# Kernel tuning notes

Hardware: AMD Instinct MI355X
Metric: run time of the kernel (lower is better)

## Reference

```python
import jax, jax.numpy as jnp
import numpy as np

N = 100000   # nodes
E = 1600000  # edges (avg degree 16)
F = 64       # input feature dim
H = 64       # hidden dim
O = 64       # conv output dim
C = 2        # channels (x.shape[1])
S = 1000     # number of subgraphs
M = 64       # nodes per subgraph
MH = 128     # MLP hidden
OUT = 1      # MLP output


def setup_inputs() -> dict:
    key = jax.random.key(0)
    ks = jax.random.split(key, 16)
    x = jax.random.normal(ks[0], (N, C, F), jnp.float32)
    edge_index = jax.random.randint(ks[1], (2, E), 0, N, dtype=jnp.int32)
    edge_weight = jax.random.uniform(ks[2], (E,), jnp.float32)
    subG_node = jax.random.randint(ks[3], (S, M), 0, N, dtype=jnp.int32)
    s1 = 1.0 / np.sqrt(F)
    s2 = 1.0 / np.sqrt(H)
    sm1 = 1.0 / np.sqrt(O)
    sm2 = 1.0 / np.sqrt(MH)
    return {
        "x": x,
        "edge_index": edge_index,
        "edge_weight": edge_weight,
        "subG_node": subG_node,
        "W1": jax.random.normal(ks[4], (F, H), jnp.float32) * s1,
        "b1": jnp.zeros((H,), jnp.float32),
        "gn_w": jnp.ones((H,), jnp.float32),
        "gn_b": jnp.zeros((H,), jnp.float32),
        "gn_ms": jnp.ones((H,), jnp.float32),
        "W2": jax.random.normal(ks[5], (H, O), jnp.float32) * s2,
        "b2": jnp.zeros((O,), jnp.float32),
        "mW1": jax.random.normal(ks[6], (O, MH), jnp.float32) * sm1,
        "mb1": jnp.zeros((MH,), jnp.float32),
        "mW2": jax.random.normal(ks[7], (MH, OUT), jnp.float32) * sm2,
        "mb2": jnp.zeros((OUT,), jnp.float32),
    }


def _graph_norm(h, w, b, ms, eps=1e-5):
    # PyG GraphNorm over all nodes (single graph): per-feature stats
    mean = jnp.mean(h, axis=0, keepdims=True)
    out = h - ms * mean
    var = jnp.mean(out * out, axis=0, keepdims=True)
    return w * out * jax.lax.rsqrt(var + eps) + b


def _gcn_layer(h, src, dst, norm, self_norm, W, b, n):
    # GCNConv: h' = D^-1/2 (A + I) D^-1/2 (h @ W) + b
    hw = h @ W                                   # [N, out]
    msg = norm[:, None] * hw[src]                # [E, out] gather
    agg = jax.ops.segment_sum(msg, dst, num_segments=n)  # scatter-add
    agg = agg + self_norm[:, None] * hw          # self-loop term
    return agg + b


def reference(x, edge_index, edge_weight, subG_node,
              W1, b1, gn_w, gn_b, gn_ms, W2, b2, mW1, mb1, mW2, mb2):
    n = x.shape[0]
    src, dst = edge_index[0], edge_index[1]
    # symmetric GCN normalization with self-loops of weight 1
    deg = jax.ops.segment_sum(edge_weight, dst, num_segments=n) + 1.0
    dinv = jax.lax.rsqrt(deg)
    norm = dinv[src] * edge_weight * dinv[dst]   # [E]
    self_norm = dinv * dinv                      # [N]

    def conv_channel(xc):  # xc: [N, F]
        h = _gcn_layer(xc, src, dst, norm, self_norm, W1, b1, n)
        h = _graph_norm(h, gn_w, gn_b, gn_ms)
        h = jax.nn.relu(h)
        return _gcn_layer(h, src, dst, norm, self_norm, W2, b2, n)

    emb = jax.vmap(conv_channel, in_axes=1, out_axes=1)(x)  # [N, C, O]
    emb = jnp.mean(emb, axis=1)                              # [N, O]
    # subgraph pooling: sp @ emb == sum of member-node embeddings
    pooled = jnp.sum(emb[subG_node], axis=1)                 # [S, O]
    h = jax.nn.relu(pooled @ mW1 + mb1)
    return h @ mW2 + mb2                                     # [S, 1]
```

## Files before the change

kernel.cpp:

```cpp
#include <hip/hip_runtime.h>
#include <hip/hip_fp16.h>

#define NNODES 100000
#define NEDGES 1600000
#define NSUB   1000
#define MSUB   64
#define MHID   128

#define WSHIFT 9
#define WIN    512
#define NWIN   ((NNODES + 511) >> 9)
#define NBLK   256
#define CHUNK  (NEDGES / NBLK)

typedef _Float16 f16x8 __attribute__((ext_vector_type(8)));
typedef float    f32x4 __attribute__((ext_vector_type(4)));


__global__ __launch_bounds__(256) void k_hist(const int* __restrict__ dst,
                                              int* __restrict__ block_counts) {
    __shared__ int hist[NWIN];
    int t = threadIdx.x, b = blockIdx.x;
    for (int i = t; i < NWIN; i += 256) hist[i] = 0;
    __syncthreads();
    int e0 = b * CHUNK;
    for (int e = e0 + t; e < e0 + CHUNK; e += 256)
        atomicAdd(&hist[dst[e] >> WSHIFT], 1);
    __syncthreads();
    for (int i = t; i < NWIN; i += 256) block_counts[b * NWIN + i] = hist[i];
}

__global__ __launch_bounds__(256) void k_winsum(const int* __restrict__ block_counts,
                                                int* __restrict__ win_total) {
    __shared__ int red[256];
    int t = threadIdx.x, w = blockIdx.x;
    red[t] = block_counts[t * NWIN + w];
    __syncthreads();
    for (int off = 128; off > 0; off >>= 1) {
        if (t < off) red[t] += red[t + off];
        __syncthreads();
    }
    if (t == 0) win_total[w] = red[0];
}

__global__ __launch_bounds__(256) void k_scan(const int* __restrict__ win_total,
                                              int* __restrict__ win_base,
                                              float* __restrict__ stats,
                                              int2* __restrict__ edges) {
    __shared__ int arr[256];
    int t = threadIdx.x;
    int own = (t < NWIN) ? win_total[t] : 0;
    arr[t] = own;
    __syncthreads();
    for (int off = 1; off < 256; off <<= 1) {
        int v = (t >= off) ? arr[t - off] : 0;
        __syncthreads();
        arr[t] += v;
        __syncthreads();
    }
    if (t < NWIN) win_base[t] = arr[t] - own;
    if (t == NWIN - 1) win_base[NWIN] = arr[t];
    stats[t] = 0.0f; stats[t + 256] = 0.0f;
    if (t < 16) edges[NEDGES + t] = make_int2(0, 0);
}

__global__ __launch_bounds__(64) void k_scan2(const int* __restrict__ block_counts,
                                              const int* __restrict__ win_base,
                                              int* __restrict__ block_off) {
    int w = blockIdx.x, lane = threadIdx.x;
    int c[4];
    int lsum = 0;
    #pragma unroll
    for (int i = 0; i < 4; i++) {
        c[i] = block_counts[(lane * 4 + i) * NWIN + w];
        lsum += c[i];
    }
    int incl = lsum;
    #pragma unroll
    for (int off = 1; off < 64; off <<= 1) {
        int u = __shfl_up(incl, off, 64);
        if (lane >= off) incl += u;
    }
    int run = win_base[w] + incl - lsum;
    #pragma unroll
    for (int i = 0; i < 4; i++) {
        block_off[(lane * 4 + i) * NWIN + w] = run;
        run += c[i];
    }
}

__global__ __launch_bounds__(256) void k_scatter(const int* __restrict__ src,
                                                 const int* __restrict__ dst,
                                                 const float* __restrict__ ew,
                                                 const int* __restrict__ block_off,
                                                 int2* __restrict__ esw) {
    __shared__ int myoff[NWIN];
    int t = threadIdx.x, b = blockIdx.x;
    for (int i = t; i < NWIN; i += 256) myoff[i] = block_off[b * NWIN + i];
    __syncthreads();
    int e0 = b * CHUNK;
    for (int e = e0 + t; e < e0 + CHUNK; e += 256) {
        int d = dst[e];
        int w = d >> WSHIFT;
        int pos = atomicAdd(&myoff[w], 1);
        int dl = d - (w << WSHIFT);
        esw[pos] = make_int2((dl << 17) | src[e], __float_as_int(ew[e]));
    }
}

__global__ __launch_bounds__(256) void k_fill2(const int* __restrict__ win_base,
                                               const int2* __restrict__ esw,
                                               int2* __restrict__ edges,
                                               int* __restrict__ row_ptr,
                                               int* __restrict__ cnt,
                                               float* __restrict__ dinv) {
    __shared__ int   cnt_l[WIN];
    __shared__ int   sc[WIN];
    __shared__ int   fill_l[WIN];
    __shared__ float degw[WIN];
    int t = threadIdx.x, w = blockIdx.x;
    #pragma unroll
    for (int i = t; i < WIN; i += 256) { cnt_l[i] = 0; fill_l[i] = 0; degw[i] = 0.f; }
    __syncthreads();
    int e0 = win_base[w], e1 = win_base[w + 1];
    for (int e = e0 + t; e < e1; e += 256) {
        int2 v = esw[e];
        int dl = ((unsigned)v.x) >> 17;
        atomicAdd(&cnt_l[dl], 1);
        atomicAdd(&degw[dl], __int_as_float(v.y));
    }
    __syncthreads();
    sc[t] = cnt_l[t]; sc[t + 256] = cnt_l[t + 256];
    __syncthreads();
    for (int off = 1; off < WIN; off <<= 1) {
        int v0 = (t >= off) ? sc[t - off] : 0;
        int v1 = (t + 256 >= off) ? sc[t + 256 - off] : 0;
        __syncthreads();
        sc[t] += v0; sc[t + 256] += v1;
        __syncthreads();
    }
    sc[t]       = e0 + sc[t]       - cnt_l[t];
    sc[t + 256] = e0 + sc[t + 256] - cnt_l[t + 256];
    __syncthreads();
    for (int e = e0 + t; e < e1; e += 256) {
        int2 v = esw[e];
        int dl = ((unsigned)v.x) >> 17;
        int pos = sc[dl] + atomicAdd(&fill_l[dl], 1);
        edges[pos] = make_int2(v.x & 0x1FFFF, v.y);
    }
    __syncthreads();
    #pragma unroll
    for (int i = t; i < WIN; i += 256) {
        int node = (w << WSHIFT) + i;
        if (node < NNODES) {
            row_ptr[node] = sc[i];
            cnt[node]     = cnt_l[i];
            dinv[node]    = rsqrtf(degw[i] + 1.0f);
        }
    }
}


template <bool TR>
__global__ __launch_bounds__(256) void k_gemm(const void* __restrict__ Xv,
                                              const float* __restrict__ Wg,
                                              const float* __restrict__ dinv,
                                              _Float16* __restrict__ Y,
                                              const float* __restrict__ Acoef,
                                              const float* __restrict__ Bcoef) {
    __shared__ __align__(16) _Float16 ob[4][16 * 72];
    int t = threadIdx.x;
    int wave = t >> 6, lane = t & 63;
    int m = lane & 15, q = lane >> 4;

    f16x8 bf[2][4];
    #pragma unroll
    for (int kb = 0; kb < 2; kb++)
        #pragma unroll
        for (int nt = 0; nt < 4; nt++)
            #pragma unroll
            for (int j = 0; j < 8; j++)
                bf[kb][nt][j] = (_Float16)Wg[(kb * 32 + q * 8 + j) * 64 + nt * 16 + m];

    float ca[16], cb[16];
    if constexpr (TR) {
        int c = m & 1;
        #pragma unroll
        for (int kb = 0; kb < 2; kb++)
            #pragma unroll
            for (int j = 0; j < 8; j++) {
                int k = kb * 32 + q * 8 + j;
                ca[kb * 8 + j] = Acoef[c * 64 + k];
                cb[kb * 8 + j] = Bcoef[c * 64 + k];
            }
    }

    int tile = blockIdx.x * 4 + wave;
    int row0 = tile * 16;

    f16x8 af[2];
    if constexpr (!TR) {
        const float* xp = (const float*)Xv + (size_t)(row0 + m) * 64;
        #pragma unroll
        for (int kb = 0; kb < 2; kb++) {
            float4 u0 = *(const float4*)(xp + kb * 32 + q * 8);
            float4 u1 = *(const float4*)(xp + kb * 32 + q * 8 + 4);
            af[kb][0] = (_Float16)u0.x; af[kb][1] = (_Float16)u0.y;
            af[kb][2] = (_Float16)u0.z; af[kb][3] = (_Float16)u0.w;
            af[kb][4] = (_Float16)u1.x; af[kb][5] = (_Float16)u1.y;
            af[kb][6] = (_Float16)u1.z; af[kb][7] = (_Float16)u1.w;
        }
    } else {
        const _Float16* xp = (const _Float16*)Xv + (size_t)(row0 + m) * 64;
        #pragma unroll
        for (int kb = 0; kb < 2; kb++) {
            f16x8 v = *(const f16x8*)(xp + kb * 32 + q * 8);
            #pragma unroll
            for (int j = 0; j < 8; j++) {
                float f = (float)v[j];
                f = fmaxf(ca[kb * 8 + j] * f + cb[kb * 8 + j], 0.0f);
                af[kb][j] = (_Float16)f;
            }
        }
    }

    f32x4 acc[4];
    #pragma unroll
    for (int nt = 0; nt < 4; nt++) {
        acc[nt] = (f32x4){0.f, 0.f, 0.f, 0.f};
        acc[nt] = __builtin_amdgcn_mfma_f32_16x16x32_f16(af[0], bf[0][nt], acc[nt], 0, 0, 0);
        acc[nt] = __builtin_amdgcn_mfma_f32_16x16x32_f16(af[1], bf[1][nt], acc[nt], 0, 0, 0);
    }

    float dv[4];
    #pragma unroll
    for (int i = 0; i < 4; i++) dv[i] = dinv[(row0 + q * 4 + i) >> 1];

    _Float16* obw = ob[wave];
    #pragma unroll
    for (int nt = 0; nt < 4; nt++)
        #pragma unroll
        for (int i = 0; i < 4; i++)
            obw[(q * 4 + i) * 72 + nt * 16 + m] = (_Float16)(acc[nt][i] * dv[i]);
    __syncthreads();

    _Float16* yp = Y + (size_t)row0 * 64;
    #pragma unroll
    for (int s = 0; s < 2; s++) {
        int c8 = s * 64 + lane;
        int r = c8 >> 3, cg = c8 & 7;
        uint4 v = *(const uint4*)(obw + r * 72 + cg * 8);
        *(uint4*)(yp + (size_t)r * 64 + cg * 8) = v;
    }
}


__global__ __launch_bounds__(256) void k_prop(const __half* __restrict__ hw,
                                              const float* __restrict__ bias,
                                              const float* __restrict__ dinv,
                                              const int* __restrict__ row_ptr,
                                              const int* __restrict__ cnt,
                                              const int2* __restrict__ edges,
                                              __half* __restrict__ agg) {
    int t = threadIdx.x;
    int lane = t & 63;
    int n = __builtin_amdgcn_readfirstlane(blockIdx.x * 4 + (t >> 6));
    if (n >= NNODES) return;

    int f = lane * 2;
    int feat = f & 63;

    float2 bv = *(const float2*)(bias + feat);
    float dv = dinv[n];
    float2 self = __half22float2(*(const __half2*)(hw + (size_t)n * 128 + f));
    float acc0 = self.x;
    float acc1 = self.y;

    int start = row_ptr[n];
    int cn    = cnt[n];
    const unsigned long long* pp = (const unsigned long long*)(edges + start);

    for (int p = 0; p < cn; p += 16) {
        unsigned long long e[16];
        #pragma unroll
        for (int i = 0; i < 16; i++) e[i] = __builtin_nontemporal_load(pp + p + i);
        float2 h[16];
        #pragma unroll
        for (int i = 0; i < 16; i++) {
            int s = (int)(e[i] & 0x1FFFFu);
            h[i] = __half22float2(*(const __half2*)(hw + (size_t)s * 128 + f));
        }
        #pragma unroll
        for (int i = 0; i < 16; i++) {
            float w = ((p + i) < cn) ? __int_as_float((int)(e[i] >> 32)) : 0.0f;
            acc0 += w * h[i].x;
            acc1 += w * h[i].y;
        }
    }

    *(__half2*)(agg + (size_t)n * 128 + f) =
        __floats2half2_rn(dv * acc0 + bv.x, dv * acc1 + bv.y);
}


__global__ __launch_bounds__(256) void k_stats(const __half* __restrict__ agg,
                                               float* __restrict__ stats) {
    __shared__ float ls[16][128];
    __shared__ float lq[16][128];
    int t = threadIdx.x;
    int cb = (t & 15) * 8;
    int rg = t >> 4;
    float s[8], q[8];
    #pragma unroll
    for (int i = 0; i < 8; i++) { s[i] = 0.f; q[i] = 0.f; }
    for (int r = blockIdx.x * 16 + rg; r < NNODES; r += gridDim.x * 16) {
        uint4 u = *(const uint4*)(agg + (size_t)r * 128 + cb);
        const __half2* h2 = (const __half2*)&u;
        #pragma unroll
        for (int i = 0; i < 4; i++) {
            float2 v = __half22float2(h2[i]);
            s[2*i]   += v.x; q[2*i]   += v.x * v.x;
            s[2*i+1] += v.y; q[2*i+1] += v.y * v.y;
        }
    }
    #pragma unroll
    for (int i = 0; i < 8; i++) { ls[rg][cb + i] = s[i]; lq[rg][cb + i] = q[i]; }
    __syncthreads();
    if (t < 128) {
        float a = 0.f, b = 0.f;
        #pragma unroll
        for (int g = 0; g < 16; g++) { a += ls[g][t]; b += lq[g][t]; }
        atomicAdd(&stats[t], a);
        atomicAdd(&stats[128 + t], b);
    }
}

__global__ void k_coef(float* stats, const float* __restrict__ gn_w,
                       const float* __restrict__ gn_b, const float* __restrict__ gn_ms) {
    int col = threadIdx.x;
    float inv_n = 1.0f / (float)NNODES;
    float mean = stats[col] * inv_n;
    float eh2  = stats[128 + col] * inv_n;
    int f = col & 63;
    float ms = gn_ms[f];
    float var = eh2 - 2.0f * ms * mean * mean + ms * ms * mean * mean;
    float A = gn_w[f] * rsqrtf(var + 1e-5f);
    stats[256 + col] = A;
    stats[384 + col] = gn_b[f] - A * ms * mean;
}


__global__ __launch_bounds__(128) void k_head(const __half* __restrict__ agg,
                                              const int* __restrict__ subg,
                                              const float* __restrict__ mW1,
                                              const float* __restrict__ mb1,
                                              const float* __restrict__ mW2,
                                              const float* __restrict__ mb2,
                                              float* __restrict__ out) {
    __shared__ float pl[128];
    __shared__ float red[128];
    int s = blockIdx.x, t = threadIdx.x;
    int j = t & 63, half = t >> 6;
    const int* idx = subg + s * 64;
    float acc = 0.f;
    for (int m = half * 32; m < half * 32 + 32; m++) {
        int n = idx[m];
        acc += 0.5f * (__half2float(agg[(size_t)n * 128 + j]) +
                       __half2float(agg[(size_t)n * 128 + 64 + j]));
    }
    pl[half * 64 + j] = acc;
    __syncthreads();
    if (t < 64) pl[t] += pl[64 + t];
    __syncthreads();
    float h = mb1[t];
    #pragma unroll
    for (int k = 0; k < 64; k++) h += pl[k] * mW1[k * 128 + t];
    h = fmaxf(h, 0.0f);
    red[t] = h * mW2[t];
    __syncthreads();
    for (int off = 64; off > 0; off >>= 1) {
        if (t < off) red[t] += red[t + off];
        __syncthreads();
    }
    if (t == 0) out[s] = red[0] + mb2[0];
}


extern "C" void kernel_launch(void* const* d_in, const int* in_sizes, int n_in,
                              void* d_out, int out_size, void* d_ws, size_t ws_size,
                              hipStream_t stream) {
    const float* x     = (const float*)d_in[0];
    const int*   ei    = (const int*)d_in[1];
    const float* ew    = (const float*)d_in[2];
    const int*   subg  = (const int*)d_in[3];
    const float* W1    = (const float*)d_in[4];
    const float* b1    = (const float*)d_in[5];
    const float* gn_w  = (const float*)d_in[6];
    const float* gn_b  = (const float*)d_in[7];
    const float* gn_ms = (const float*)d_in[8];
    const float* W2    = (const float*)d_in[9];
    const float* b2    = (const float*)d_in[10];
    const float* mW1   = (const float*)d_in[11];
    const float* mb1   = (const float*)d_in[12];
    const float* mW2   = (const float*)d_in[13];
    const float* mb2   = (const float*)d_in[14];
    float* out = (float*)d_out;

    char* w = (char*)d_ws;
    size_t off = 0;
    auto alloc = [&](size_t bytes) {
        void* p = w + off;
        off = (off + bytes + 255) & ~(size_t)255;
        return p;
    };
    float*  dinv      = (float*) alloc((size_t)NNODES * 4);
    int*    cnt       = (int*)   alloc((size_t)NNODES * 4);
    int*    row_ptr   = (int*)   alloc((size_t)NNODES * 4);
    int2*   edges     = (int2*)  alloc(((size_t)NEDGES + 16) * 8);
    int2*   esw       = (int2*)  alloc((size_t)NEDGES * 8);
    __half* hw        = (__half*)alloc((size_t)NNODES * 128 * 2);
    __half* agg       = (__half*)alloc((size_t)NNODES * 128 * 2);
    float*  stats     = (float*) alloc(512 * 4);
    int*    block_counts = (int*)alloc((size_t)NBLK * NWIN * 4);
    int*    block_off    = (int*)alloc((size_t)NBLK * NWIN * 4);
    int*    win_total    = (int*)alloc(NWIN * 4);
    int*    win_base     = (int*)alloc((NWIN + 1) * 4);

    const int* src = ei;
    const int* dst = ei + NEDGES;

    k_hist   <<<NBLK, 256, 0, stream>>>(dst, block_counts);
    k_winsum <<<NWIN, 256, 0, stream>>>(block_counts, win_total);
    k_scan   <<<1, 256, 0, stream>>>(win_total, win_base, stats, edges);
    k_scan2  <<<NWIN, 64, 0, stream>>>(block_counts, win_base, block_off);
    k_scatter<<<NBLK, 256, 0, stream>>>(src, dst, ew, block_off, esw);
    k_fill2  <<<NWIN, 256, 0, stream>>>(win_base, esw, edges, row_ptr, cnt, dinv);

    k_gemm<false><<<3125, 256, 0, stream>>>(x, W1, dinv, (_Float16*)hw, nullptr, nullptr);
    k_prop<<<25000, 256, 0, stream>>>(hw, b1, dinv, row_ptr, cnt, edges, agg);

    k_stats<<<512, 256, 0, stream>>>(agg, stats);
    k_coef<<<1, 128, 0, stream>>>(stats, gn_w, gn_b, gn_ms);

    k_gemm<true><<<3125, 256, 0, stream>>>(agg, W2, dinv, (_Float16*)hw, stats + 256, stats + 384);
    k_prop<<<25000, 256, 0, stream>>>(hw, b2, dinv, row_ptr, cnt, edges, agg);

    k_head<<<NSUB, 128, 0, stream>>>(agg, subg, mW1, mb1, mW2, mb2, out);
}
```

Measured before the change: 382.9 us.

## Pack edges into 32-bit with quantized weights and merge offset kernels

```diff
diff --git a/kernel.cpp b/kernel.cpp
--- a/kernel.cpp
+++ b/kernel.cpp
@@ -18,9 +18,11 @@
 
 
 __global__ __launch_bounds__(256) void k_hist(const int* __restrict__ dst,
-                                              int* __restrict__ block_counts) {
+                                              int* __restrict__ block_counts,
+                                              int* __restrict__ cursor) {
     __shared__ int hist[NWIN];
     int t = threadIdx.x, b = blockIdx.x;
+    if (b == 0 && t == 0) *cursor = 0;
     for (int i = t; i < NWIN; i += 256) hist[i] = 0;
     __syncthreads();
     int e0 = b * CHUNK;
@@ -30,62 +32,37 @@
     for (int i = t; i < NWIN; i += 256) block_counts[b * NWIN + i] = hist[i];
 }
 
-__global__ __launch_bounds__(256) void k_winsum(const int* __restrict__ block_counts,
-                                                int* __restrict__ win_total) {
+__global__ __launch_bounds__(256) void k_off(const int* __restrict__ block_counts,
+                                             int* __restrict__ cursor,
+                                             int* __restrict__ win_base,
+                                             int* __restrict__ win_lim,
+                                             int* __restrict__ block_off,
+                                             float* __restrict__ stats,
+                                             unsigned* __restrict__ edges) {
+    __shared__ int arr[256];
     __shared__ int red[256];
+    __shared__ int base_s;
     int t = threadIdx.x, w = blockIdx.x;
-    red[t] = block_counts[t * NWIN + w];
+    int own = block_counts[t * NWIN + w];
+    arr[t] = own; red[t] = own;
     __syncthreads();
     for (int off = 128; off > 0; off >>= 1) {
         if (t < off) red[t] += red[t + off];
         __syncthreads();
     }
-    if (t == 0) win_total[w] = red[0];
-}
-
-__global__ __launch_bounds__(256) void k_scan(const int* __restrict__ win_total,
-                                              int* __restrict__ win_base,
-                                              float* __restrict__ stats,
-                                              int2* __restrict__ edges) {
-    __shared__ int arr[256];
-    int t = threadIdx.x;
-    int own = (t < NWIN) ? win_total[t] : 0;
-    arr[t] = own;
-    __syncthreads();
+    if (t == 0) base_s = atomicAdd(cursor, red[0]);
     for (int off = 1; off < 256; off <<= 1) {
         int v = (t >= off) ? arr[t - off] : 0;
         __syncthreads();
         arr[t] += v;
         __syncthreads();
     }
-    if (t < NWIN) win_base[t] = arr[t] - own;
-    if (t == NWIN - 1) win_base[NWIN] = arr[t];
-    stats[t] = 0.0f; stats[t + 256] = 0.0f;
-    if (t < 16) edges[NEDGES + t] = make_int2(0, 0);
-}
-
-__global__ __launch_bounds__(64) void k_scan2(const int* __restrict__ block_counts,
-                                              const int* __restrict__ win_base,
-                                              int* __restrict__ block_off) {
-    int w = blockIdx.x, lane = threadIdx.x;
-    int c[4];
-    int lsum = 0;
-    #pragma unroll
-    for (int i = 0; i < 4; i++) {
-        c[i] = block_counts[(lane * 4 + i) * NWIN + w];
-        lsum += c[i];
-    }
-    int incl = lsum;
-    #pragma unroll
-    for (int off = 1; off < 64; off <<= 1) {
-        int u = __shfl_up(incl, off, 64);
-        if (lane >= off) incl += u;
-    }
-    int run = win_base[w] + incl - lsum;
-    #pragma unroll
-    for (int i = 0; i < 4; i++) {
-        block_off[(lane * 4 + i) * NWIN + w] = run;
-        run += c[i];
+    int base = base_s;
+    block_off[t * NWIN + w] = base + arr[t] - own;
+    if (t == 0) { win_base[w] = base; win_lim[w] = base + red[0]; }
+    if (w == 0) {
+        stats[t] = 0.0f; stats[t + 256] = 0.0f;
+        if (t < 16) edges[NEDGES + t] = 0u;
     }
 }
 
@@ -109,8 +86,9 @@
 }
 
 __global__ __launch_bounds__(256) void k_fill2(const int* __restrict__ win_base,
+                                               const int* __restrict__ win_lim,
                                                const int2* __restrict__ esw,
-                                               int2* __restrict__ edges,
+                                               unsigned* __restrict__ edges,
                                                int* __restrict__ row_ptr,
                                                int* __restrict__ cnt,
                                                float* __restrict__ dinv) {
@@ -122,7 +100,7 @@
     #pragma unroll
     for (int i = t; i < WIN; i += 256) { cnt_l[i] = 0; fill_l[i] = 0; degw[i] = 0.f; }
     __syncthreads();
-    int e0 = win_base[w], e1 = win_base[w + 1];
+    int e0 = win_base[w], e1 = win_lim[w];
     for (int e = e0 + t; e < e1; e += 256) {
         int2 v = esw[e];
         int dl = ((unsigned)v.x) >> 17;
@@ -146,7 +124,8 @@
         int2 v = esw[e];
         int dl = ((unsigned)v.x) >> 17;
         int pos = sc[dl] + atomicAdd(&fill_l[dl], 1);
-        edges[pos] = make_int2(v.x & 0x1FFFF, v.y);
+        int wq = __float2int_rn(__int_as_float(v.y) * 32767.0f);
+        edges[pos] = ((unsigned)wq << 17) | ((unsigned)v.x & 0x1FFFFu);
     }
     __syncthreads();
     #pragma unroll
@@ -166,8 +145,10 @@
                                               const float* __restrict__ Wg,
                                               const float* __restrict__ dinv,
                                               _Float16* __restrict__ Y,
-                                              const float* __restrict__ Acoef,
-                                              const float* __restrict__ Bcoef) {
+                                              const float* __restrict__ stats,
+                                              const float* __restrict__ gn_w,
+                                              const float* __restrict__ gn_b,
+                                              const float* __restrict__ gn_ms) {
     __shared__ __align__(16) _Float16 ob[4][16 * 72];
     int t = threadIdx.x;
     int wave = t >> 6, lane = t & 63;
@@ -185,13 +166,21 @@
     float ca[16], cb[16];
     if constexpr (TR) {
         int c = m & 1;
+        const float inv_n = 1.0f / (float)NNODES;
         #pragma unroll
         for (int kb = 0; kb < 2; kb++)
             #pragma unroll
             for (int j = 0; j < 8; j++) {
                 int k = kb * 32 + q * 8 + j;
-                ca[kb * 8 + j] = Acoef[c * 64 + k];
-                cb[kb * 8 + j] = Bcoef[c * 64 + k];
+                int col = c * 64 + k;
+                float mean = stats[col] * inv_n;
+                float eh2  = stats[128 + col] * inv_n;
+                float ms   = gn_ms[k];
+                float mm   = ms * mean;
+                float var  = eh2 - 2.0f * mm * mean + mm * mm;
+                float A = gn_w[k] * rsqrtf(var + 1e-5f);
+                ca[kb * 8 + j] = A;
+                cb[kb * 8 + j] = gn_b[k] - A * mm;
             }
     }
 
@@ -260,7 +249,7 @@
                                               const float* __restrict__ dinv,
                                               const int* __restrict__ row_ptr,
                                               const int* __restrict__ cnt,
-                                              const int2* __restrict__ edges,
+                                              const unsigned* __restrict__ edges,
                                               __half* __restrict__ agg) {
     int t = threadIdx.x;
     int lane = t & 63;
@@ -269,6 +258,7 @@
 
     int f = lane * 2;
     int feat = f & 63;
+    const float qs = 1.0f / 32767.0f;
 
     float2 bv = *(const float2*)(bias + feat);
     float dv = dinv[n];
@@ -278,12 +268,14 @@
 
     int start = row_ptr[n];
     int cn    = cnt[n];
-    const unsigned long long* pp = (const unsigned long long*)(edges + start);
-
-    for (int p = 0; p < cn; p += 16) {
-        unsigned long long e[16];
-        #pragma unroll
-        for (int i = 0; i < 16; i++) e[i] = __builtin_nontemporal_load(pp + p + i);
+    const unsigned* pp = edges + start;
+
+    int full = cn & ~15;
+    int p = 0;
+    for (; p < full; p += 16) {
+        unsigned e[16];
+        #pragma unroll
+        for (int i = 0; i < 16; i++) e[i] = pp[p + i];
         float2 h[16];
         #pragma unroll
         for (int i = 0; i < 16; i++) {
@@ -292,7 +284,24 @@
         }
         #pragma unroll
         for (int i = 0; i < 16; i++) {
-            float w = ((p + i) < cn) ? __int_as_float((int)(e[i] >> 32)) : 0.0f;
+            float w = (float)(e[i] >> 17) * qs;
+            acc0 += w * h[i].x;
+            acc1 += w * h[i].y;
+        }
+    }
+    if (p < cn) {
+        unsigned e[16];
+        #pragma unroll
+        for (int i = 0; i < 16; i++) e[i] = pp[p + i];
+        float2 h[16];
+        #pragma unroll
+        for (int i = 0; i < 16; i++) {
+            int s = (int)(e[i] & 0x1FFFFu);
+            h[i] = __half22float2(*(const __half2*)(hw + (size_t)s * 128 + f));
+        }
+        #pragma unroll
+        for (int i = 0; i < 16; i++) {
+            float w = ((p + i) < cn) ? (float)(e[i] >> 17) * qs : 0.0f;
             acc0 += w * h[i].x;
             acc1 += w * h[i].y;
         }
@@ -335,48 +344,39 @@
     }
 }
 
-__global__ void k_coef(float* stats, const float* __restrict__ gn_w,
-                       const float* __restrict__ gn_b, const float* __restrict__ gn_ms) {
-    int col = threadIdx.x;
-    float inv_n = 1.0f / (float)NNODES;
-    float mean = stats[col] * inv_n;
-    float eh2  = stats[128 + col] * inv_n;
-    int f = col & 63;
-    float ms = gn_ms[f];
-    float var = eh2 - 2.0f * ms * mean * mean + ms * ms * mean * mean;
-    float A = gn_w[f] * rsqrtf(var + 1e-5f);
-    stats[256 + col] = A;
-    stats[384 + col] = gn_b[f] - A * ms * mean;
-}
-
-
-__global__ __launch_bounds__(128) void k_head(const __half* __restrict__ agg,
+
+__global__ __launch_bounds__(256) void k_head(const __half* __restrict__ agg,
                                               const int* __restrict__ subg,
                                               const float* __restrict__ mW1,
                                               const float* __restrict__ mb1,
                                               const float* __restrict__ mW2,
                                               const float* __restrict__ mb2,
                                               float* __restrict__ out) {
-    __shared__ float pl[128];
+    __shared__ int   idx[64];
+    __shared__ float pl[4][64];
     __shared__ float red[128];
     int s = blockIdx.x, t = threadIdx.x;
-    int j = t & 63, half = t >> 6;
-    const int* idx = subg + s * 64;
+    if (t < 64) idx[t] = subg[s * 64 + t];
+    __syncthreads();
+    int j = t & 63, grp = t >> 6;
     float acc = 0.f;
-    for (int m = half * 32; m < half * 32 + 32; m++) {
+    #pragma unroll
+    for (int m = grp * 16; m < grp * 16 + 16; m++) {
         int n = idx[m];
-        acc += 0.5f * (__half2float(agg[(size_t)n * 128 + j]) +
-                       __half2float(agg[(size_t)n * 128 + 64 + j]));
-    }
-    pl[half * 64 + j] = acc;
-    __syncthreads();
-    if (t < 64) pl[t] += pl[64 + t];
-    __syncthreads();
-    float h = mb1[t];
-    #pragma unroll
-    for (int k = 0; k < 64; k++) h += pl[k] * mW1[k * 128 + t];
-    h = fmaxf(h, 0.0f);
-    red[t] = h * mW2[t];
+        acc += __half2float(agg[(size_t)n * 128 + j]) +
+               __half2float(agg[(size_t)n * 128 + 64 + j]);
+    }
+    pl[grp][j] = acc * 0.5f;
+    __syncthreads();
+    if (t < 64) pl[0][t] = pl[0][t] + pl[1][t] + pl[2][t] + pl[3][t];
+    __syncthreads();
+    if (t < 128) {
+        float h = mb1[t];
+        #pragma unroll
+        for (int k = 0; k < 64; k++) h += pl[0][k] * mW1[k * 128 + t];
+        h = fmaxf(h, 0.0f);
+        red[t] = h * mW2[t];
+    }
     __syncthreads();
     for (int off = 64; off > 0; off >>= 1) {
         if (t < off) red[t] += red[t + off];
@@ -413,37 +413,38 @@
         off = (off + bytes + 255) & ~(size_t)255;
         return p;
     };
-    float*  dinv      = (float*) alloc((size_t)NNODES * 4);
-    int*    cnt       = (int*)   alloc((size_t)NNODES * 4);
-    int*    row_ptr   = (int*)   alloc((size_t)NNODES * 4);
-    int2*   edges     = (int2*)  alloc(((size_t)NEDGES + 16) * 8);
-    int2*   esw       = (int2*)  alloc((size_t)NEDGES * 8);
-    __half* hw        = (__half*)alloc((size_t)NNODES * 128 * 2);
-    __half* agg       = (__half*)alloc((size_t)NNODES * 128 * 2);
-    float*  stats     = (float*) alloc(512 * 4);
-    int*    block_counts = (int*)alloc((size_t)NBLK * NWIN * 4);
-    int*    block_off    = (int*)alloc((size_t)NBLK * NWIN * 4);
-    int*    win_total    = (int*)alloc(NWIN * 4);
-    int*    win_base     = (int*)alloc((NWIN + 1) * 4);
+    float*    dinv    = (float*)   alloc((size_t)NNODES * 4);
+    int*      cnt     = (int*)     alloc((size_t)NNODES * 4);
+    int*      row_ptr = (int*)     alloc((size_t)NNODES * 4);
+    unsigned* edges   = (unsigned*)alloc(((size_t)NEDGES + 16) * 4);
+    int2*     esw     = (int2*)    alloc((size_t)NEDGES * 8);
+    __half*   hw      = (__half*)  alloc((size_t)NNODES * 128 * 2);
+    __half*   agg     = (__half*)  alloc((size_t)NNODES * 128 * 2);
+    float*    stats   = (float*)   alloc(512 * 4);
+    int*      block_counts = (int*)alloc((size_t)NBLK * NWIN * 4);
+    int*      block_off    = (int*)alloc((size_t)NBLK * NWIN * 4);
+    int*      win_base     = (int*)alloc(NWIN * 4);
+    int*      win_lim      = (int*)alloc(NWIN * 4);
+    int*      cursor       = (int*)alloc(256);
 
     const int* src = ei;
     const int* dst = ei + NEDGES;
 
-    k_hist   <<<NBLK, 256, 0, stream>>>(dst, block_counts);
-    k_winsum <<<NWIN, 256, 0, stream>>>(block_counts, win_total);
-    k_scan   <<<1, 256, 0, stream>>>(win_total, win_base, stats, edges);
-    k_scan2  <<<NWIN, 64, 0, stream>>>(block_counts, win_base, block_off);
+    k_hist   <<<NBLK, 256, 0, stream>>>(dst, block_counts, cursor);
+    k_off    <<<NWIN, 256, 0, stream>>>(block_counts, cursor, win_base, win_lim,
+                                        block_off, stats, edges);
     k_scatter<<<NBLK, 256, 0, stream>>>(src, dst, ew, block_off, esw);
-    k_fill2  <<<NWIN, 256, 0, stream>>>(win_base, esw, edges, row_ptr, cnt, dinv);
-
-    k_gemm<false><<<3125, 256, 0, stream>>>(x, W1, dinv, (_Float16*)hw, nullptr, nullptr);
+    k_fill2  <<<NWIN, 256, 0, stream>>>(win_base, win_lim, esw, edges, row_ptr, cnt, dinv);
+
+    k_gemm<false><<<3125, 256, 0, stream>>>(x, W1, dinv, (_Float16*)hw,
+                                            nullptr, nullptr, nullptr, nullptr);
     k_prop<<<25000, 256, 0, stream>>>(hw, b1, dinv, row_ptr, cnt, edges, agg);
 
     k_stats<<<512, 256, 0, stream>>>(agg, stats);
-    k_coef<<<1, 128, 0, stream>>>(stats, gn_w, gn_b, gn_ms);
-
-    k_gemm<true><<<3125, 256, 0, stream>>>(agg, W2, dinv, (_Float16*)hw, stats + 256, stats + 384);
+
+    k_gemm<true><<<3125, 256, 0, stream>>>(agg, W2, dinv, (_Float16*)hw,
+                                           stats, gn_w, gn_b, gn_ms);
     k_prop<<<25000, 256, 0, stream>>>(hw, b2, dinv, row_ptr, cnt, edges, agg);
 
-    k_head<<<NSUB, 128, 0, stream>>>(agg, subg, mW1, mb1, mW2, mb2, out);
-}
+    k_head<<<NSUB, 256, 0, stream>>>(agg, subg, mW1, mb1, mW2, mb2, out);
+}
```

Result: faster. 354.6 us (-7.4%).
